# Performance work log

Measured on AMD Instinct MI355X. Metric: run time of the kernel, lower is better.

Reference implementation:

```python
import jax, jax.numpy as jnp
import numpy as np

N, E, IN, H = 50000, 800000, 128, 2
C1, C2 = 64, 32  # conv1 per-head channels = 2*out_channels, mu/logstd per-head = out_channels
NEG_SLOPE = 0.2


def setup_inputs() -> dict:
    key = jax.random.key(0)
    ks = jax.random.split(key, 16)
    x = jax.random.normal(ks[0], (N, IN), jnp.float32)
    src = jax.random.randint(ks[1], (E,), 0, N)
    dst = jax.random.randint(ks[2], (E,), 0, N)
    dst = jnp.where(src == dst, (dst + 1) % N, dst)  # data has no self loops
    edge_index = jnp.stack([src, dst]).astype(jnp.int64)

    def glorot(k, shape, fan_in):
        return jax.random.normal(k, shape, jnp.float32) * np.float32(1.0 / np.sqrt(fan_in))

    return {
        "x": x,
        "edge_index": edge_index,
        "W1": glorot(ks[3], (IN, H * C1), IN),
        "att_l1": glorot(ks[4], (H, C1), C1),
        "att_r1": glorot(ks[5], (H, C1), C1),
        "b1": jnp.zeros((H * C1,), jnp.float32),
        "Wmu": glorot(ks[6], (H * C1, H * C2), H * C1),
        "att_lmu": glorot(ks[7], (H, C2), C2),
        "att_rmu": glorot(ks[8], (H, C2), C2),
        "bmu": jnp.zeros((H * C2,), jnp.float32),
        "Wls": glorot(ks[9], (H * C1, H * C2), H * C1),
        "att_lls": glorot(ks[10], (H, C2), C2),
        "att_rls": glorot(ks[11], (H, C2), C2),
        "bls": jnp.zeros((H * C2,), jnp.float32),
    }


def supergat_layer(x, W, att_l, att_r, b, src, dst, heads, ch):
    """SuperGATConv ('MX', concat=True) inference forward."""
    n = x.shape[0]
    h = (x @ W).reshape(n, heads, ch)          # [N,H,C]
    hi = h[dst]                                # x_i (target), [E,H,C]
    hj = h[src]                                # x_j (source), [E,H,C]
    logits = jnp.sum(hi * hj, axis=-1)         # [E,H] dot-product logits
    alpha = jnp.sum(hj * att_l, axis=-1) + jnp.sum(hi * att_r, axis=-1)
    alpha = alpha * jax.nn.sigmoid(logits)
    alpha = jax.nn.leaky_relu(alpha, NEG_SLOPE)
    # segment softmax over destination neighborhoods (self loops => no empty segments)
    amax = jax.ops.segment_max(alpha, dst, num_segments=n)
    ea = jnp.exp(alpha - amax[dst])
    denom = jax.ops.segment_sum(ea, dst, num_segments=n)
    alpha = ea / (denom[dst] + 1e-16)
    out = jax.ops.segment_sum(hj * alpha[..., None], dst, num_segments=n)  # [N,H,C]
    return out.reshape(n, heads * ch) + b


def reference(x, edge_index, W1, att_l1, att_r1, b1, Wmu, att_lmu, att_rmu, bmu, Wls, att_lls, att_rls, bls):
    n = x.shape[0]
    loop = jnp.arange(n, dtype=edge_index.dtype)
    src = jnp.concatenate([edge_index[0], loop])
    dst = jnp.concatenate([edge_index[1], loop])
    h = jax.nn.elu(supergat_layer(x, W1, att_l1, att_r1, b1, src, dst, H, C1))
    mu = supergat_layer(h, Wmu, att_lmu, att_rmu, bmu, src, dst, H, C2)
    logstd = supergat_layer(h, Wls, att_lls, att_rls, bls, src, dst, H, C2)
    return (mu, logstd)
```

## Files before the change

### kernel.cpp

```cpp
#include <hip/hip_runtime.h>
#include <math.h>

#define N_NODES 50000
#define N_EDGES 800000
#define ETOT    (N_EDGES + N_NODES)
#define GEMM_TILES ((N_NODES + 63) / 64)
#define NROWS 50048
#define TROWS 65536
#define SENT_ROW 65535
#define NPART 8
#define PART_SIZE (N_NODES / NPART)
#define CHUNK_EDGES 2048
#define NCHUNK ((ETOT + CHUNK_EDGES - 1) / CHUNK_EDGES)

typedef _Float16 f16x8 __attribute__((ext_vector_type(8)));
typedef _Float16 f16x4 __attribute__((ext_vector_type(4)));
typedef _Float16 f16x2 __attribute__((ext_vector_type(2)));
typedef float    f32x4 __attribute__((ext_vector_type(4)));


__device__ __forceinline__ void scatter_body(int sbid, const int* __restrict__ ei,
                                             int* __restrict__ fillArr,
                                             unsigned short* __restrict__ srcs) {
    int part = sbid & (NPART - 1);
    int chunk = sbid >> 3;
    int lo = part * PART_SIZE, hi = lo + PART_SIZE;
    int base = chunk * CHUNK_EDGES + threadIdx.x;
#pragma unroll
    for (int it = 0; it < CHUNK_EDGES / 256; ++it) {
        int e = base + it * 256;
        if (e >= ETOT) break;
        int d = (e < N_EDGES) ? ei[N_EDGES + e] : (e - N_EDGES);
        if (d >= lo && d < hi) {
            int s = (e < N_EDGES) ? ei[e] : d;
            int pos = (d << 6) + (atomicAdd(&fillArr[d], 1) + 1);
            srcs[pos] = (unsigned short)s;
        }
    }
}


__device__ __forceinline__ void stage_B_rows1(const float* __restrict__ B0,
                                              _Float16* B, int t) {
#pragma unroll
    for (int it = 0; it < 16; ++it) {
        int id = it * 256 + t;
        int k = id >> 5, c4 = id & 31;
        float4 v = ((const float4*)B0)[id];
        _Float16* d = &B[k * 128 + c4 * 4];
        d[0] = (_Float16)v.x; d[1] = (_Float16)v.y;
        d[2] = (_Float16)v.z; d[3] = (_Float16)v.w;
    }
}

__device__ __forceinline__ void stage_B_rows2(const float* __restrict__ B0,
                                              const float* __restrict__ B1,
                                              _Float16* B, int t) {
#pragma unroll
    for (int it = 0; it < 8; ++it) {
        int id = it * 256 + t;
        int k = id >> 4, c4 = id & 15;
        float4 v = ((const float4*)B0)[id];
        _Float16* d = &B[k * 128 + c4 * 4];
        d[0] = (_Float16)v.x; d[1] = (_Float16)v.y;
        d[2] = (_Float16)v.z; d[3] = (_Float16)v.w;
        float4 w = ((const float4*)B1)[id];
        _Float16* e2 = &B[k * 128 + 64 + c4 * 4];
        e2[0] = (_Float16)w.x; e2[1] = (_Float16)w.y;
        e2[2] = (_Float16)w.z; e2[3] = (_Float16)w.w;
    }
}

__device__ __forceinline__ void transpose_swz(_Float16* B, int t) {
    __syncthreads();
    f16x8 g[8];
#pragma unroll
    for (int it = 0; it < 8; ++it) {
        int id = it * 256 + t;
        int n = id >> 4, gk = id & 15;
#pragma unroll
        for (int j = 0; j < 8; ++j) g[it][j] = B[(gk * 8 + j) * 128 + n];
    }
    __syncthreads();
#pragma unroll
    for (int it = 0; it < 8; ++it) {
        int id = it * 256 + t;
        int n = id >> 4, gk = id & 15;
        int gs = gk ^ (n & 7);
        *(f16x8*)&B[n * 128 + gs * 8] = g[it];
    }
    __syncthreads();
}

__device__ __forceinline__ void mfma_tile(const f16x8 a[4], const _Float16* Bt,
                                          f32x4 acc[8], int l) {
    int i16 = l & 15, q = l >> 4;
#pragma unroll
    for (int tt = 0; tt < 8; ++tt) acc[tt] = (f32x4){0.f, 0.f, 0.f, 0.f};
#pragma unroll
    for (int kb = 0; kb < 4; ++kb) {
#pragma unroll
        for (int tt = 0; tt < 8; ++tt) {
            int n = tt * 16 + i16;
            int gs = (kb * 4 + q) ^ (n & 7);
            f16x8 b = *(const f16x8*)&Bt[n * 128 + gs * 8];
            acc[tt] = __builtin_amdgcn_mfma_f32_16x16x32_f16(a[kb], b, acc[tt], 0, 0, 0);
        }
    }
}

__device__ __forceinline__ void store_C(const f32x4 acc[8], _Float16* cs,
                                        _Float16* __restrict__ C, int r0, int l) {
    int i16 = l & 15, q = l >> 4;
#pragma unroll
    for (int tt = 0; tt < 8; ++tt)
#pragma unroll
        for (int r = 0; r < 4; ++r)
            cs[(q * 4 + r) * 128 + tt * 16 + i16] = (_Float16)acc[tt][r];
#pragma unroll
    for (int u = 0; u < 4; ++u) {
        int idx = u * 64 + l;
        int rr = idx >> 4, cc = idx & 15;
        f16x8 v = ((f16x8*)cs)[idx];
        if (r0 + rr >= N_NODES) v = (f16x8)(_Float16)0.f;
        ((f16x8*)(C + (size_t)(r0 + rr) * 128))[cc] = v;
    }
}

__global__ void __launch_bounds__(256) g1s_k(const float* __restrict__ A,
                                             const float* __restrict__ B0,
                                             const float* __restrict__ att_l,
                                             const float* __restrict__ att_r,
                                             _Float16* __restrict__ C,
                                             float* __restrict__ al,
                                             float* __restrict__ ar,
                                             const int* __restrict__ ei,
                                             int* __restrict__ fillArr,
                                             unsigned short* __restrict__ srcs) {
    __shared__ _Float16 Bsh[128 * 128];
    __shared__ _Float16 Cst[4][16 * 128];
    if (blockIdx.x >= GEMM_TILES) {
        scatter_body(blockIdx.x - GEMM_TILES, ei, fillArr, srcs);
        return;
    }
    int t = threadIdx.x;
    stage_B_rows1(B0, Bsh, t);
    transpose_swz(Bsh, t);
    int wave = t >> 6, l = t & 63;
    int i16 = l & 15, q = l >> 4;
    float attL[8], attR[8];
#pragma unroll
    for (int tt = 0; tt < 8; ++tt) {
        int col = tt * 16 + i16;
        attL[tt] = att_l[col];
        attR[tt] = att_r[col];
    }
    int r0 = blockIdx.x * 64 + wave * 16;
    const float* ar_ = A + (size_t)min(r0 + i16, N_NODES - 1) * 128;
    f16x8 a[4];
#pragma unroll
    for (int kb = 0; kb < 4; ++kb) {
        float4 u = ((const float4*)(ar_ + kb * 32 + q * 8))[0];
        float4 v = ((const float4*)(ar_ + kb * 32 + q * 8))[1];
        f16x8 t8;
        t8[0] = (_Float16)u.x; t8[1] = (_Float16)u.y;
        t8[2] = (_Float16)u.z; t8[3] = (_Float16)u.w;
        t8[4] = (_Float16)v.x; t8[5] = (_Float16)v.y;
        t8[6] = (_Float16)v.z; t8[7] = (_Float16)v.w;
        a[kb] = t8;
    }
    f32x4 acc[8];
    mfma_tile(a, Bsh, acc, l);
    store_C(acc, &Cst[wave][0], C, r0, l);
    float pl[2][4], pr[2][4];
#pragma unroll
    for (int h = 0; h < 2; ++h)
#pragma unroll
        for (int r = 0; r < 4; ++r) {
            float sl = 0.f, sr = 0.f;
#pragma unroll
            for (int k = 0; k < 4; ++k) {
                float v = acc[h * 4 + k][r];
                sl += v * attL[h * 4 + k];
                sr += v * attR[h * 4 + k];
            }
            pl[h][r] = sl; pr[h][r] = sr;
        }
#pragma unroll
    for (int m = 1; m < 16; m <<= 1) {
#pragma unroll
        for (int h = 0; h < 2; ++h)
#pragma unroll
            for (int r = 0; r < 4; ++r) {
                pl[h][r] += __shfl_xor(pl[h][r], m);
                pr[h][r] += __shfl_xor(pr[h][r], m);
            }
    }
    if (i16 == 0) {
#pragma unroll
        for (int h = 0; h < 2; ++h)
#pragma unroll
            for (int r = 0; r < 4; ++r) {
                int row = r0 + q * 4 + r;
                al[row * 2 + h] = pl[h][r];
                ar[row * 2 + h] = pr[h][r];
            }
    }
    if (blockIdx.x == 0) {
        if (t < 16) ((f16x8*)(C + (size_t)SENT_ROW * 128))[t] = (f16x8)(_Float16)0.f;
        else if (t == 16) {
            al[SENT_ROW * 2] = -1e30f; al[SENT_ROW * 2 + 1] = -1e30f;
            ar[SENT_ROW * 2] = 0.f;    ar[SENT_ROW * 2 + 1] = 0.f;
        }
    }
}

__global__ void __launch_bounds__(256) gemm2_k(const _Float16* __restrict__ A,
                                               const float* __restrict__ B0,
                                               const float* __restrict__ B1,
                                               const float* __restrict__ attlmu,
                                               const float* __restrict__ attrmu,
                                               const float* __restrict__ attlls,
                                               const float* __restrict__ attrls,
                                               _Float16* __restrict__ C,
                                               float* __restrict__ alc,
                                               float* __restrict__ arc) {
    __shared__ _Float16 Bsh[128 * 128];
    __shared__ _Float16 Cst[4][16 * 128];
    int t = threadIdx.x;
    stage_B_rows2(B0, B1, Bsh, t);
    transpose_swz(Bsh, t);
    int wave = t >> 6, l = t & 63;
    int i16 = l & 15, q = l >> 4;
    float attL[8], attR[8];
#pragma unroll
    for (int tt = 0; tt < 8; ++tt) {
        int col = tt * 16 + i16;
        const float* la = (tt < 4) ? attlmu : attlls;
        const float* ra = (tt < 4) ? attrmu : attrls;
        attL[tt] = la[col & 63];
        attR[tt] = ra[col & 63];
    }
    int r0 = blockIdx.x * 64 + wave * 16;
    const _Float16* ar_ = A + (size_t)min(r0 + i16, N_NODES - 1) * 128;
    f16x8 a[4];
#pragma unroll
    for (int kb = 0; kb < 4; ++kb)
        a[kb] = *(const f16x8*)(ar_ + kb * 32 + q * 8);
    f32x4 acc[8];
    mfma_tile(a, Bsh, acc, l);
    store_C(acc, &Cst[wave][0], C, r0, l);
    float pl[4][4], pr[4][4];
#pragma unroll
    for (int g = 0; g < 4; ++g)
#pragma unroll
        for (int r = 0; r < 4; ++r) {
            float sl = 0.f, sr = 0.f;
#pragma unroll
            for (int k = 0; k < 2; ++k) {
                float v = acc[g * 2 + k][r];
                sl += v * attL[g * 2 + k];
                sr += v * attR[g * 2 + k];
            }
            pl[g][r] = sl; pr[g][r] = sr;
        }
#pragma unroll
    for (int m = 1; m < 16; m <<= 1) {
#pragma unroll
        for (int g = 0; g < 4; ++g)
#pragma unroll
            for (int r = 0; r < 4; ++r) {
                pl[g][r] += __shfl_xor(pl[g][r], m);
                pr[g][r] += __shfl_xor(pr[g][r], m);
            }
    }
    if (i16 == 0) {
#pragma unroll
        for (int g = 0; g < 4; ++g)
#pragma unroll
            for (int r = 0; r < 4; ++r) {
                int row = r0 + q * 4 + r;
                alc[row * 4 + g] = pl[g][r];
                arc[row * 4 + g] = pr[g][r];
            }
    }
    if (blockIdx.x == 0) {
        if (t < 16) ((f16x8*)(C + (size_t)SENT_ROW * 128))[t] = (f16x8)(_Float16)0.f;
        else if (t == 16) {
#pragma unroll
            for (int g = 0; g < 4; ++g) {
                alc[SENT_ROW * 4 + g] = -1e30f;
                arc[SENT_ROW * 4 + g] = 0.f;
            }
        }
    }
}


__device__ __forceinline__ float sigmoidf_fast(float x) {
    return 1.f / (1.f + __expf(-x));
}

__device__ __forceinline__ float dot8_f16(f16x8 a, f16x8 b) {
    float part = 0.f;
#if __has_builtin(__builtin_amdgcn_fdot2)
    f16x2* pa = (f16x2*)&a;
    f16x2* pb = (f16x2*)&b;
#pragma unroll
    for (int kk = 0; kk < 4; ++kk)
        part = __builtin_amdgcn_fdot2(pa[kk], pb[kk], part, false);
#else
#pragma unroll
    for (int kk = 0; kk < 8; ++kk) part += (float)a[kk] * (float)b[kk];
#endif
    return part;
}

__device__ __forceinline__ float leaky_clamp(float x) {
    return __builtin_amdgcn_fmed3f(x, 0.2f * x, 60.f);
}

__global__ void __launch_bounds__(256) edge1_k(const _Float16* __restrict__ h1,
                                               const float* __restrict__ al,
                                               const float* __restrict__ ar,
                                               const int* __restrict__ fillArr,
                                               const unsigned short* __restrict__ srcs,
                                               const float* __restrict__ b1,
                                               _Float16* __restrict__ h2o) {
    int i = (blockIdx.x * blockDim.x + threadIdx.x) >> 6;
    int l = threadIdx.x & 63;
    if (i >= N_NODES) return;
    int c16 = l & 7;
    int head = c16 >> 2;
    int sub = l >> 3;

    const f16x8* rowi = (const f16x8*)(h1 + (size_t)i * 128);
    f16x8 hiA = rowi[c16 * 2], hiB = rowi[c16 * 2 + 1];
    float ari = ar[i * 2 + head];
    int cnt = fillArr[i] + 1;
    int start = i << 6;
    int n = (cnt + 7) >> 3;
    int n3 = n / 3;
    int rem = n - n3 * 3;

    float s = 0.f;
    float o[16];
#pragma unroll
    for (int k = 0; k < 16; ++k) o[k] = 0.f;

    int p = start + sub;
    f16x8 qA0, qB0, qA1, qB1, qA2, qB2;
    float a0, a1, a2;

#define LOADE1(QA, QB, AA)                                              \
    {                                                                   \
        int j_ = srcs[p]; p += 8;                                       \
        const f16x8* rp_ = (const f16x8*)(h1 + (size_t)j_ * 128);       \
        QA = rp_[c16 * 2]; QB = rp_[c16 * 2 + 1];                       \
        AA = al[j_ * 2 + head];                                         \
    }

#define CONS1(QA, QB, AA)                                               \
    {                                                                   \
        float part_ = dot8_f16(hiA, QA) + dot8_f16(hiB, QB);            \
        part_ += __shfl_xor(part_, 1);                                  \
        part_ += __shfl_xor(part_, 2);                                  \
        float a_ = (AA + ari) * sigmoidf_fast(part_);                   \
        float w_ = __expf(leaky_clamp(a_));                             \
        s += w_;                                                        \
        _Pragma("unroll")                                               \
        for (int k = 0; k < 8; ++k) o[k] += w_ * (float)QA[k];          \
        _Pragma("unroll")                                               \
        for (int k = 0; k < 8; ++k) o[8 + k] += w_ * (float)QB[k];      \
    }

    LOADE1(qA0, qB0, a0);
    LOADE1(qA1, qB1, a1);
    LOADE1(qA2, qB2, a2);

    for (int gg = 0; gg < n3; ++gg) {
        CONS1(qA0, qB0, a0); LOADE1(qA0, qB0, a0);
        CONS1(qA1, qB1, a1); LOADE1(qA1, qB1, a1);
        CONS1(qA2, qB2, a2); LOADE1(qA2, qB2, a2);
    }
    if (rem > 0) CONS1(qA0, qB0, a0);
    if (rem > 1) CONS1(qA1, qB1, a1);

#undef LOADE1
#undef CONS1

#pragma unroll
    for (int m = 8; m < 64; m <<= 1) {
        s += __shfl_xor(s, m);
#pragma unroll
        for (int k = 0; k < 16; ++k) o[k] += __shfl_xor(o[k], m);
    }
    if (l < 8) {
        float inv = 1.f / (s + 1e-16f);
        f16x8 rA, rB;
#pragma unroll
        for (int k = 0; k < 16; ++k) {
            float r = o[k] * inv + b1[l * 16 + k];
            r = (r > 0.f) ? r : (__expf(r) - 1.f);
            if (k < 8) rA[k] = (_Float16)r; else rB[k - 8] = (_Float16)r;
        }
        f16x8* dst = (f16x8*)(h2o + (size_t)i * 128);
        dst[l * 2] = rA;
        dst[l * 2 + 1] = rB;
    }
}

__global__ void __launch_bounds__(256) edge23_k(const _Float16* __restrict__ hcat,
                                                const float* __restrict__ alc,
                                                const float* __restrict__ arc,
                                                const int* __restrict__ fillArr,
                                                const unsigned short* __restrict__ srcs,
                                                const float* __restrict__ bmu,
                                                const float* __restrict__ bls,
                                                float* __restrict__ out) {
    int i = (blockIdx.x * blockDim.x + threadIdx.x) >> 6;
    int l = threadIdx.x & 63;
    if (i >= N_NODES) return;
    int c16 = l & 7;
    int g = c16 >> 1;
    int sub = l >> 3;

    const f16x8* rowi = (const f16x8*)(hcat + (size_t)i * 128);
    f16x8 hiA = rowi[c16 * 2], hiB = rowi[c16 * 2 + 1];
    float ari = arc[i * 4 + g];
    int cnt = fillArr[i] + 1;
    int start = i << 6;
    int n = (cnt + 7) >> 3;
    int n3 = n / 3;
    int rem = n - n3 * 3;

    float s = 0.f;
    float o[16];
#pragma unroll
    for (int k = 0; k < 16; ++k) o[k] = 0.f;

    int p = start + sub;
    f16x8 qA0, qB0, qA1, qB1, qA2, qB2;
    float a0, a1, a2;

#define LOADE2(QA, QB, AA)                                              \
    {                                                                   \
        int j_ = srcs[p]; p += 8;                                       \
        const f16x8* rp_ = (const f16x8*)(hcat + (size_t)j_ * 128);     \
        QA = rp_[c16 * 2]; QB = rp_[c16 * 2 + 1];                       \
        AA = alc[j_ * 4 + g];                                           \
    }

#define CONS2(QA, QB, AA)                                               \
    {                                                                   \
        float part_ = dot8_f16(hiA, QA) + dot8_f16(hiB, QB);            \
        part_ += __shfl_xor(part_, 1);                                  \
        float a_ = (AA + ari) * sigmoidf_fast(part_);                   \
        float w_ = __expf(leaky_clamp(a_));                             \
        s += w_;                                                        \
        _Pragma("unroll")                                               \
        for (int k = 0; k < 8; ++k) o[k] += w_ * (float)QA[k];          \
        _Pragma("unroll")                                               \
        for (int k = 0; k < 8; ++k) o[8 + k] += w_ * (float)QB[k];      \
    }

    LOADE2(qA0, qB0, a0);
    LOADE2(qA1, qB1, a1);
    LOADE2(qA2, qB2, a2);

    for (int gg = 0; gg < n3; ++gg) {
        CONS2(qA0, qB0, a0); LOADE2(qA0, qB0, a0);
        CONS2(qA1, qB1, a1); LOADE2(qA1, qB1, a1);
        CONS2(qA2, qB2, a2); LOADE2(qA2, qB2, a2);
    }
    if (rem > 0) CONS2(qA0, qB0, a0);
    if (rem > 1) CONS2(qA1, qB1, a1);

#undef LOADE2
#undef CONS2

#pragma unroll
    for (int m = 8; m < 64; m <<= 1) {
        s += __shfl_xor(s, m);
#pragma unroll
        for (int k = 0; k < 16; ++k) o[k] += __shfl_xor(o[k], m);
    }
    if (l < 8) {
        float inv = 1.f / (s + 1e-16f);
        int br = l >> 2;
        int cIn = (l & 3) * 16;
        const float* b = br ? bls : bmu;
        float* dst = out + (size_t)br * (N_NODES * 64) + (size_t)i * 64 + cIn;
#pragma unroll
        for (int v4 = 0; v4 < 4; ++v4) {
            float4 bv = ((const float4*)(b + cIn))[v4];
            float4 r;
            r.x = o[v4 * 4 + 0] * inv + bv.x;
            r.y = o[v4 * 4 + 1] * inv + bv.y;
            r.z = o[v4 * 4 + 2] * inv + bv.z;
            r.w = o[v4 * 4 + 3] * inv + bv.w;
            ((float4*)dst)[v4] = r;
        }
    }
}


extern "C" void kernel_launch(void* const* d_in, const int* in_sizes, int n_in,
                              void* d_out, int out_size, void* d_ws, size_t ws_size,
                              hipStream_t stream) {
    const float* x      = (const float*)d_in[0];
    const int*   ei     = (const int*)d_in[1];
    const float* W1     = (const float*)d_in[2];
    const float* att_l1 = (const float*)d_in[3];
    const float* att_r1 = (const float*)d_in[4];
    const float* b1     = (const float*)d_in[5];
    const float* Wmu    = (const float*)d_in[6];
    const float* attlmu = (const float*)d_in[7];
    const float* attrmu = (const float*)d_in[8];
    const float* bmu    = (const float*)d_in[9];
    const float* Wls    = (const float*)d_in[10];
    const float* attlls = (const float*)d_in[11];
    const float* attrls = (const float*)d_in[12];
    const float* bls    = (const float*)d_in[13];
    float* out = (float*)d_out;

    _Float16* h1   = (_Float16*)d_ws;
    _Float16* hcat = h1 + (size_t)TROWS * 128;
    _Float16* h2   = hcat + (size_t)TROWS * 128;
    float* al1   = (float*)(h2 + (size_t)NROWS * 128);
    float* ar1   = al1 + TROWS * 2;
    float* alc   = ar1 + TROWS * 2;
    float* arc   = alc + TROWS * 4;
    int* fillArr = (int*)(arc + TROWS * 4);
    unsigned short* srcs = (unsigned short*)(fillArr + 50048);

    hipMemsetAsync(fillArr, 0xFF, 50048 * sizeof(int) + 3200128 * sizeof(unsigned short),
                   stream);

    g1s_k<<<GEMM_TILES + NCHUNK * NPART, 256, 0, stream>>>(x, W1, att_l1, att_r1,
                                                           h1, al1, ar1,
                                                           ei, fillArr, srcs);

    int nblocks = (N_NODES + 3) / 4;
    edge1_k<<<nblocks, 256, 0, stream>>>(h1, al1, ar1, fillArr, srcs, b1, h2);

    gemm2_k<<<GEMM_TILES, 256, 0, stream>>>(h2, Wmu, Wls, attlmu, attrmu, attlls, attrls,
                                            hcat, alc, arc);
    edge23_k<<<nblocks, 256, 0, stream>>>(hcat, alc, arc, fillArr, srcs, bmu, bls, out);
}
```

Before: 273.7 us.

## Split fused scatter/GEMM1 kernel and swizzle B staging to avoid LDS conflicts

Splits the combined GEMM1-plus-edge-scatter launch back into two separate kernels, a scatter kernel and a GEMM1 kernel, run back to back on the stream. It also XOR-swizzles the row-major fp16 staging of the weight matrix in shared memory so the column-wise transpose reads hit different banks. The split removes the divergent branch and the large shared-memory allocation from scatter blocks, which may let more of them be resident at once. In exchange it loses the overlap between the GEMM and the scatter and adds one more kernel launch.

```diff
diff --git a/kernel.cpp b/kernel.cpp
--- a/kernel.cpp
+++ b/kernel.cpp
@@ -19,11 +19,11 @@
 typedef float    f32x4 __attribute__((ext_vector_type(4)));
 
 
-__device__ __forceinline__ void scatter_body(int sbid, const int* __restrict__ ei,
-                                             int* __restrict__ fillArr,
-                                             unsigned short* __restrict__ srcs) {
-    int part = sbid & (NPART - 1);
-    int chunk = sbid >> 3;
+__global__ void __launch_bounds__(256) scatter_k(const int* __restrict__ ei,
+                                                 int* __restrict__ fillArr,
+                                                 unsigned short* __restrict__ srcs) {
+    int part = blockIdx.x & (NPART - 1);
+    int chunk = blockIdx.x >> 3;
     int lo = part * PART_SIZE, hi = lo + PART_SIZE;
     int base = chunk * CHUNK_EDGES + threadIdx.x;
 #pragma unroll
@@ -47,7 +47,7 @@
         int id = it * 256 + t;
         int k = id >> 5, c4 = id & 31;
         float4 v = ((const float4*)B0)[id];
-        _Float16* d = &B[k * 128 + c4 * 4];
+        _Float16* d = &B[k * 128 + (((c4 >> 1) ^ (k >> 3)) << 3) + (c4 & 1) * 4];
         d[0] = (_Float16)v.x; d[1] = (_Float16)v.y;
         d[2] = (_Float16)v.z; d[3] = (_Float16)v.w;
     }
@@ -61,11 +61,11 @@
         int id = it * 256 + t;
         int k = id >> 4, c4 = id & 15;
         float4 v = ((const float4*)B0)[id];
-        _Float16* d = &B[k * 128 + c4 * 4];
+        _Float16* d = &B[k * 128 + (((c4 >> 1) ^ (k >> 3)) << 3) + (c4 & 1) * 4];
         d[0] = (_Float16)v.x; d[1] = (_Float16)v.y;
         d[2] = (_Float16)v.z; d[3] = (_Float16)v.w;
         float4 w = ((const float4*)B1)[id];
-        _Float16* e2 = &B[k * 128 + 64 + c4 * 4];
+        _Float16* e2 = &B[k * 128 + (((8 + (c4 >> 1)) ^ (k >> 3)) << 3) + (c4 & 1) * 4];
         e2[0] = (_Float16)w.x; e2[1] = (_Float16)w.y;
         e2[2] = (_Float16)w.z; e2[3] = (_Float16)w.w;
     }
@@ -79,7 +79,8 @@
         int id = it * 256 + t;
         int n = id >> 4, gk = id & 15;
 #pragma unroll
-        for (int j = 0; j < 8; ++j) g[it][j] = B[(gk * 8 + j) * 128 + n];
+        for (int j = 0; j < 8; ++j)
+            g[it][j] = B[(gk * 8 + j) * 128 + (((n >> 3) ^ gk) << 3) + (n & 7)];
     }
     __syncthreads();
 #pragma unroll
@@ -127,22 +128,15 @@
     }
 }
 
-__global__ void __launch_bounds__(256) g1s_k(const float* __restrict__ A,
-                                             const float* __restrict__ B0,
-                                             const float* __restrict__ att_l,
-                                             const float* __restrict__ att_r,
-                                             _Float16* __restrict__ C,
-                                             float* __restrict__ al,
-                                             float* __restrict__ ar,
-                                             const int* __restrict__ ei,
-                                             int* __restrict__ fillArr,
-                                             unsigned short* __restrict__ srcs) {
+__global__ void __launch_bounds__(256) gemm1_k(const float* __restrict__ A,
+                                               const float* __restrict__ B0,
+                                               const float* __restrict__ att_l,
+                                               const float* __restrict__ att_r,
+                                               _Float16* __restrict__ C,
+                                               float* __restrict__ al,
+                                               float* __restrict__ ar) {
     __shared__ _Float16 Bsh[128 * 128];
     __shared__ _Float16 Cst[4][16 * 128];
-    if (blockIdx.x >= GEMM_TILES) {
-        scatter_body(blockIdx.x - GEMM_TILES, ei, fillArr, srcs);
-        return;
-    }
     int t = threadIdx.x;
     stage_B_rows1(B0, Bsh, t);
     transpose_swz(Bsh, t);
@@ -537,9 +531,9 @@
     hipMemsetAsync(fillArr, 0xFF, 50048 * sizeof(int) + 3200128 * sizeof(unsigned short),
                    stream);
 
-    g1s_k<<<GEMM_TILES + NCHUNK * NPART, 256, 0, stream>>>(x, W1, att_l1, att_r1,
-                                                           h1, al1, ar1,
-                                                           ei, fillArr, srcs);
+    scatter_k<<<NCHUNK * NPART, 256, 0, stream>>>(ei, fillArr, srcs);
+
+    gemm1_k<<<GEMM_TILES, 256, 0, stream>>>(x, W1, att_l1, att_r1, h1, al1, ar1);
 
     int nblocks = (N_NODES + 3) / 4;
     edge1_k<<<nblocks, 256, 0, stream>>>(h1, al1, ar1, fillArr, srcs, b1, h2);
```

New measurement: 262.1 us. 1.04x faster.
